# Kernel tuning notes

Measured on AMD Instinct MI355X. Metric: run time of the kernel, lower is better.

## Reference

```python
import jax, jax.numpy as jnp
import numpy as np

NUM_CLASSES = 7
B = 14336
D = 512
H_KDE = 0.2          # sklearn KernelDensity(bandwidth=0.2, kernel='gaussian')
KERNEL_MUL = 2.0
KERNEL_NUM = 5
BN_EPS = 1e-5


def _pairwise_sqdist(a, b):
    # ||a_i - b_j||^2 via gram trick; avoids the [n,n,d] broadcast tensor the torch code builds
    an = jnp.sum(a * a, axis=-1)
    bn = jnp.sum(b * b, axis=-1)
    d2 = an[:, None] + bn[None, :] - 2.0 * (a @ b.T)
    return jnp.maximum(d2, 0.0)


def _multi_kernel(total):
    # sum of KERNEL_NUM Gaussian kernels, bandwidths 1.25 * 2^i (bandwidth=5 / 2^(5//2))
    d2 = _pairwise_sqdist(total, total)
    bw0 = 5.0 / (KERNEL_MUL ** (KERNEL_NUM // 2))
    k = jnp.zeros_like(d2)
    for i in range(KERNEL_NUM):  # small fixed loop, avoids [5,n,n] intermediate
        k = k + jnp.exp(-d2 / (bw0 * (KERNEL_MUL ** i)))
    return k


def _mmd(src, tgt):
    m = src.shape[0]
    k = _multi_kernel(jnp.concatenate([src, tgt], axis=0))
    return jnp.mean(k[:m, :m] + k[m:, m:] - k[:m, m:] - k[m:, :m])


def _kde_weight(class_feats):
    # sklearn gaussian KDE: log p(x_i) = logsumexp_j(-||x_i-x_j||^2 / (2 h^2)) - log m - (d/2) log(2 pi h^2)
    # volume v = sum_i 1 / log p(x_i); weight = 1 / (v + 1e-5)
    C, m, d = class_feats.shape
    log_norm = -0.5 * d * jnp.log(2.0 * jnp.pi * (H_KDE ** 2)) - jnp.log(jnp.float32(m))

    def one(f):
        d2 = _pairwise_sqdist(f, f)
        logp = jax.nn.logsumexp(-d2 / (2.0 * (H_KDE ** 2)), axis=1) + log_norm
        return jnp.sum(1.0 / logp)

    v = jax.vmap(one)(class_feats)
    return 1.0 / (v + 1e-5)


def setup_inputs() -> dict:
    key = jax.random.key(0)
    k1, k2 = jax.random.split(key)
    fea = jax.random.normal(k1, (B, D), dtype=jnp.float32) * 0.05
    W_fc = jax.random.normal(k2, (NUM_CLASSES, D), dtype=jnp.float32) * 0.02
    gamma = jnp.ones((NUM_CLASSES,), dtype=jnp.float32)
    beta = jnp.zeros((NUM_CLASSES,), dtype=jnp.float32)
    # balanced, contiguous class blocks so per-class splits are static reshapes
    targets = jnp.repeat(jnp.arange(NUM_CLASSES, dtype=jnp.int32), B // NUM_CLASSES)
    return {"fea": fea, "W_fc": W_fc, "gamma": gamma, "beta": beta, "targets": targets}


def reference(fea, W_fc, gamma, beta, targets):
    Bn, d = fea.shape
    C = NUM_CLASSES
    m = Bn // C

    # out = BatchNorm1d(fc(fea)) in train mode (biased batch stats)
    logits = fea @ W_fc.T                              # [B, C]
    mu = jnp.mean(logits, axis=0)
    var = jnp.var(logits, axis=0)
    out = gamma * (logits - mu) / jnp.sqrt(var + BN_EPS) + beta

    # split_feature_makeLD with balanced contiguous targets -> static reshape
    cf = fea.reshape(C, m, d)                          # [C, m, D]

    # KDE density weights: computed on detached numpy features in the original -> stop_gradient
    w = jax.lax.stop_gradient(_kde_weight(cf))         # [C]

    def per_class(i):
        src = cf[i]
        # remove_element concatenates classes 0..i-1, i+1..C-1 in order;
        # first m rows of that = class 0 (class 1 when i == 0)
        tgt = cf[jnp.where(i > 0, 0, 1)]
        return _mmd(src, tgt)

    losses = jax.vmap(per_class)(jnp.arange(C))        # [C]
    affinity_loss = -jnp.sum(losses * w)
    return (out, affinity_loss)
```

## Files before the change

### kernel.cpp

```cpp
#include <hip/hip_runtime.h>

#define B_ROWS 14336
#define D_DIM  512
#define C_CLS  7
#define M_CLS  2048

typedef __attribute__((ext_vector_type(4))) float f32x4;

#define FP8_SCALE 64.0f
#define INV_2S2   (2.0f / 4096.0f)

typedef const __attribute__((address_space(1))) char gchar_t;
typedef __attribute__((address_space(3))) char lchar_t;

__device__ __forceinline__ void gload16(const char* g, char* l) {
  __builtin_amdgcn_global_load_lds((gchar_t*)g, (lchar_t*)l, 16, 0, 0);
}

__global__ __launch_bounds__(256) void k_prep(const float* __restrict__ fea,
                                              const float* __restrict__ W,
                                              char* __restrict__ f8p,
                                              float* __restrict__ an,
                                              float* __restrict__ logits,
                                              float* __restrict__ zb) {
  int t = threadIdx.x, wave = t >> 6, lane = t & 63;
  if (blockIdx.x == 0 && t < 64) zb[t] = 0.f;
  __shared__ char lrow[16 * 528];

  int r0 = blockIdx.x * 16;
#pragma unroll
  for (int k = 0; k < 4; ++k) {
    int rl = wave * 4 + k;
    int row = r0 + rl;
    const float4* fr4 = (const float4*)(fea + (size_t)row * D_DIM);
    float4 v0 = fr4[lane * 2], v1 = fr4[lane * 2 + 1];

    float p[8];
#pragma unroll
    for (int c = 0; c < 7; ++c) {
      const float4* w4 = (const float4*)(W + c * D_DIM);
      float4 q0 = w4[lane * 2], q1 = w4[lane * 2 + 1];
      p[c] = v0.x * q0.x + v0.y * q0.y + v0.z * q0.z + v0.w * q0.w +
             v1.x * q1.x + v1.y * q1.y + v1.z * q1.z + v1.w * q1.w;
    }
    p[7] = v0.x * v0.x + v0.y * v0.y + v0.z * v0.z + v0.w * v0.w +
           v1.x * v1.x + v1.y * v1.y + v1.z * v1.z + v1.w * v1.w;

#pragma unroll
    for (int c = 0; c < 8; ++c) {
      p[c] += __shfl_xor(p[c], 1);
      p[c] += __shfl_xor(p[c], 2);
      p[c] += __shfl_xor(p[c], 4);
    }
    int v = lane & 7;
    float y = p[0];
    y = (v == 1) ? p[1] : y;
    y = (v == 2) ? p[2] : y;
    y = (v == 3) ? p[3] : y;
    y = (v == 4) ? p[4] : y;
    y = (v == 5) ? p[5] : y;
    y = (v == 6) ? p[6] : y;
    y = (v == 7) ? p[7] : y;
    y += __shfl_xor(y, 8);
    y += __shfl_xor(y, 16);
    y += __shfl_xor(y, 32);
    if (lane < 7) logits[row * 7 + lane] = y;
    else if (lane == 7) an[row] = y;

    int w0 = __builtin_amdgcn_cvt_pk_fp8_f32(v0.x * FP8_SCALE, v0.y * FP8_SCALE, 0, 0);
    w0     = __builtin_amdgcn_cvt_pk_fp8_f32(v0.z * FP8_SCALE, v0.w * FP8_SCALE, w0, 1);
    int w1 = __builtin_amdgcn_cvt_pk_fp8_f32(v1.x * FP8_SCALE, v1.y * FP8_SCALE, 0, 0);
    w1     = __builtin_amdgcn_cvt_pk_fp8_f32(v1.z * FP8_SCALE, v1.w * FP8_SCALE, w1, 1);
    *(int2*)&lrow[rl * 528 + lane * 8] = make_int2(w0, w1);
  }
  __syncthreads();
  int4* outp = (int4*)f8p + (size_t)blockIdx.x * 512;
#pragma unroll
  for (int pi = 0; pi < 2; ++pi) {
    int idx = pi * 256 + t;
    int kp = idx >> 6, l = idx & 63;
    int sr = l & 15, qk = l >> 4;
    int2 lo = *(const int2*)&lrow[sr * 528 + kp * 64 + qk * 8];
    int2 hi = *(const int2*)&lrow[sr * 528 + kp * 64 + 32 + qk * 8];
    outp[idx] = make_int4(lo.x, lo.y, hi.x, hi.y);
  }
}

__global__ __launch_bounds__(256, 4) void k_gram(const char* __restrict__ f8p,
                                                 const float* __restrict__ an,
                                                 const float* __restrict__ logits,
                                                 float* __restrict__ S,
                                                 float* __restrict__ rs_part,
                                                 float* __restrict__ S1,
                                                 float* __restrict__ S2,
                                                 float* __restrict__ aff) {
  int x = blockIdx.x & 7, u = blockIdx.x >> 3;
  int t = threadIdx.x, lane = t & 63, wave = t >> 6;
  if (blockIdx.x == 0 && t == 0) aff[0] = 0.f;

  if (u >= 311) {
    int blk;
    if (u == 311) blk = x;
    else { if (x >= 6) return; blk = 8 + x; }
    int idx = blk * 4 + wave;
    int c = idx >> 3, seg = idx & 7;
    int r0 = seg * 1792;
    float s1 = 0.f, s2 = 0.f;
    for (int j = lane; j < 1792; j += 64) {
      float v = logits[(size_t)(r0 + j) * 7 + c];
      s1 += v;
      s2 += v * v;
    }
#pragma unroll
    for (int o = 1; o < 64; o <<= 1) {
      s1 += __shfl_xor(s1, o);
      s2 += __shfl_xor(s2, o);
    }
    if (lane == 0) { atomicAdd(&S1[c], s1); atomicAdd(&S2[c], s2); }
    return;
  }

  int cls1, cls2, ti, tj, Sidx;
  bool self;
  if (x < 7 && u < 136) {
    int a = 0, r = u;
    while (r > a) { r -= a + 1; ++a; }
    ti = a; tj = r;
    cls1 = x; cls2 = x; Sidx = x; self = true;
  } else {
    int j;
    if (x < 7) j = x * 175 + (u - 136);
    else j = 1225 + u;
    int p = j >> 8, t256 = j & 255;
    ti = t256 >> 4; tj = t256 & 15;
    cls1 = p + 1; cls2 = 0; Sidx = 7 + p; self = false;
  }

  __shared__ char ldsA[2][8192];
  __shared__ char ldsB[2][8192];
  __shared__ float bacc[4];

  int R0 = cls1 * 2048 + ti * 128;
  int C0 = cls2 * 2048 + tj * 128;

  const char* gA0 = f8p + ((size_t)(R0 >> 4) + wave * 2)     * 8192 + lane * 16;
  const char* gA1 = f8p + ((size_t)(R0 >> 4) + wave * 2 + 1) * 8192 + lane * 16;
  const char* gB0 = f8p + ((size_t)(C0 >> 4) + wave * 2)     * 8192 + lane * 16;
  const char* gB1 = f8p + ((size_t)(C0 >> 4) + wave * 2 + 1) * 8192 + lane * 16;

  int wr = wave >> 1, wc = wave & 1;
  int q = lane >> 4, s = lane & 15;

  f32x4 acc[4][4];
#pragma unroll
  for (int i = 0; i < 4; ++i)
#pragma unroll
    for (int j = 0; j < 4; ++j)
      acc[i][j] = (f32x4){0.f, 0.f, 0.f, 0.f};

  gload16(gA0, &ldsA[0][(wave * 2) * 1024 + lane * 16]);
  gload16(gA1, &ldsA[0][(wave * 2 + 1) * 1024 + lane * 16]);
  gload16(gB0, &ldsB[0][(wave * 2) * 1024 + lane * 16]);
  gload16(gB1, &ldsB[0][(wave * 2 + 1) * 1024 + lane * 16]);
  __syncthreads();

#define MM16(A0_, A1_, I0_, I1_)                                              \
  do {                                                                        \
    asm volatile("s_waitcnt lgkmcnt(0)" ::: "memory");                        \
    __builtin_amdgcn_sched_barrier(0);                                        \
    __builtin_amdgcn_s_setprio(1);                                            \
    _Pragma("unroll")                                                         \
    for (int j_ = 0; j_ < 4; ++j_)                                            \
      acc[I0_][j_] = __builtin_amdgcn_mfma_f32_16x16x32_fp8_fp8(              \
          A0_.x, bb[j_].x, acc[I0_][j_], 0, 0, 0);                            \
    _Pragma("unroll")                                                         \
    for (int j_ = 0; j_ < 4; ++j_)                                            \
      acc[I1_][j_] = __builtin_amdgcn_mfma_f32_16x16x32_fp8_fp8(              \
          A1_.x, bb[j_].x, acc[I1_][j_], 0, 0, 0);                            \
    _Pragma("unroll")                                                         \
    for (int j_ = 0; j_ < 4; ++j_)                                            \
      acc[I0_][j_] = __builtin_amdgcn_mfma_f32_16x16x32_fp8_fp8(              \
          A0_.y, bb[j_].y, acc[I0_][j_], 0, 0, 0);                            \
    _Pragma("unroll")                                                         \
    for (int j_ = 0; j_ < 4; ++j_)                                            \
      acc[I1_][j_] = __builtin_amdgcn_mfma_f32_16x16x32_fp8_fp8(              \
          A1_.y, bb[j_].y, acc[I1_][j_], 0, 0, 0);                            \
    __builtin_amdgcn_s_setprio(0);                                            \
  } while (0)

#pragma unroll 1
  for (int kt = 0; kt < 8; ++kt) {
    int cur = kt & 1;
    const char* LA = &ldsA[cur][(wr * 4) * 1024 + lane * 16];
    const char* LB = &ldsB[cur][(wc * 4) * 1024 + lane * 16];
    longlong2 a0, a1, bb[4];
    a0 = *(const longlong2*)(LA);
    a1 = *(const longlong2*)(LA + 1024);
#pragma unroll
    for (int j = 0; j < 4; ++j) bb[j] = *(const longlong2*)(LB + j * 1024);
    if (kt < 7) {
      int nb = cur ^ 1;
      gload16(gA0 + (kt + 1) * 1024, &ldsA[nb][(wave * 2) * 1024 + lane * 16]);
      gload16(gA1 + (kt + 1) * 1024, &ldsA[nb][(wave * 2 + 1) * 1024 + lane * 16]);
    }
    MM16(a0, a1, 0, 1);
    a0 = *(const longlong2*)(LA + 2 * 1024);
    a1 = *(const longlong2*)(LA + 3 * 1024);
    if (kt < 7) {
      int nb = cur ^ 1;
      gload16(gB0 + (kt + 1) * 1024, &ldsB[nb][(wave * 2) * 1024 + lane * 16]);
      gload16(gB1 + (kt + 1) * 1024, &ldsB[nb][(wave * 2 + 1) * 1024 + lane * 16]);
    }
    __builtin_amdgcn_s_barrier();
    asm volatile("" ::: "memory");
    MM16(a0, a1, 2, 3);
    if (kt < 7)
      asm volatile("s_waitcnt vmcnt(0)" ::: "memory");
    __builtin_amdgcn_s_barrier();
    asm volatile("" ::: "memory");
  }
#undef MM16

  bool dg = self && (ti == tj);
  bool mirror = self && (ti > tj);
  float blockAcc = 0.f;
  float colAcc[4] = {0.f, 0.f, 0.f, 0.f};
  float anB_[4];
#pragma unroll
  for (int j = 0; j < 4; ++j) anB_[j] = an[C0 + wc * 64 + j * 16 + s];

#pragma unroll
  for (int i = 0; i < 4; ++i) {
    f32x4 anA_ = *(const f32x4*)&an[R0 + wr * 64 + i * 16 + q * 4];
#pragma unroll
    for (int rg = 0; rg < 4; ++rg) {
      int rl = wr * 64 + i * 16 + q * 4 + rg;
      float aA = anA_[rg];
      float rowAcc = 0.f;
#pragma unroll
      for (int j = 0; j < 4; ++j) {
        int cl = wc * 64 + j * 16 + s;
        float g = acc[i][j][rg];
        float d2 = fmaxf(aA + anB_[j] - g * INV_2S2, 0.f);
        if (dg && rl == cl) d2 = 0.f;
        float e1 = __expf(-0.05f * d2);
        float e2 = e1 * e1, e4 = e2 * e2, e8 = e4 * e4, e16 = e8 * e8;
        blockAcc += e1 + e2 + e4 + e8 + e16;
        if (self) {
          float ek = __expf(-12.5f * d2);
          rowAcc += ek;
          if (mirror) colAcc[j] += ek;
        }
      }
      if (self) {
        rowAcc += __shfl_xor(rowAcc, 1);
        rowAcc += __shfl_xor(rowAcc, 2);
        rowAcc += __shfl_xor(rowAcc, 4);
        rowAcc += __shfl_xor(rowAcc, 8);
        if (s == 0)
          rs_part[(size_t)(R0 + rl) * 64 + tj * 2 + wc] = rowAcc;
      }
    }
  }
  if (mirror) {
#pragma unroll
    for (int j = 0; j < 4; ++j) {
      float v = colAcc[j];
      v += __shfl_xor(v, 16);
      v += __shfl_xor(v, 32);
      if (q == 0)
        rs_part[(size_t)(C0 + wc * 64 + j * 16 + s) * 64 + 32 + ti * 2 + wr] = v;
    }
    blockAcc *= 2.f;
  }
#pragma unroll
  for (int o = 1; o < 64; o <<= 1) blockAcc += __shfl_xor(blockAcc, o);
  if (lane == 0) bacc[wave] = blockAcc;
  __syncthreads();
  if (t == 0)
    atomicAdd(&S[Sidx], bacc[0] + bacc[1] + bacc[2] + bacc[3]);
}

__global__ __launch_bounds__(1024) void k_final(const float* __restrict__ logits,
                                                const float* __restrict__ S1,
                                                const float* __restrict__ S2,
                                                const float* __restrict__ gamma,
                                                const float* __restrict__ beta,
                                                const float* __restrict__ rs_part,
                                                const float* __restrict__ S,
                                                float* __restrict__ out) {
  int b = blockIdx.x, t = threadIdx.x;
  if (b < 98) {
    int idx = b * 1024 + t;
    int row = idx / 7;
    int c = idx - row * 7;
    float mu = S1[c] * (1.f / 14336.f);
    float var = S2[c] * (1.f / 14336.f) - mu * mu;
    out[idx] = gamma[c] * (logits[idx] - mu) * rsqrtf(var + 1e-5f) + beta[c];
    return;
  }
  int c = b - 98;
  const float LOG_NORM = 345.9110632f;
  float v = 0.f;
  for (int i = t; i < M_CLS; i += 1024) {
    int bi = i >> 7;
    const float* rp = rs_part + (size_t)(c * M_CLS + i) * 64;
    float rsum = 0.f;
    const float2* rpd = (const float2*)rp;
    for (int k = 0; k <= bi; ++k) {
      float2 xx = rpd[k];
      rsum += xx.x + xx.y;
    }
    const float2* rpm = (const float2*)(rp + 34 + 2 * bi);
    for (int k = 0; k < 15 - bi; ++k) {
      float2 xx = rpm[k];
      rsum += xx.x + xx.y;
    }
    v += 1.f / (logf(rsum) + LOG_NORM);
  }
#pragma unroll
  for (int o = 1; o < 64; o <<= 1) v += __shfl_xor(v, o);
  __shared__ float r[16];
  if ((t & 63) == 0) r[t >> 6] = v;
  __syncthreads();
  if (t == 0) {
    float vs = 0.f;
#pragma unroll
    for (int w = 0; w < 16; ++w) vs += r[w];
    float w = 1.f / (vs + 1e-5f);
    const float inv_m2 = 1.0f / ((float)M_CLS * (float)M_CLS);
    float Ssrc = S[c];
    float Stgt = (c > 0) ? S[0] : S[1];
    float X    = (c > 0) ? S[6 + c] : S[7];
    float mmd = (Ssrc + Stgt - 2.f * X) * inv_m2;
    atomicAdd(&out[100352], -mmd * w);
  }
}

extern "C" void kernel_launch(void* const* d_in, const int* in_sizes, int n_in,
                              void* d_out, int out_size, void* d_ws, size_t ws_size,
                              hipStream_t stream) {
  const float* fea   = (const float*)d_in[0];
  const float* W_fc  = (const float*)d_in[1];
  const float* gamma = (const float*)d_in[2];
  const float* beta  = (const float*)d_in[3];
  float* out = (float*)d_out;

  char* ws = (char*)d_ws;
  char* f8p = ws;
  float* fbase   = (float*)(ws + 7340032);
  float* an      = fbase;
  float* logits  = fbase + 14336;
  float* zb      = fbase + 114688;
  float* S1      = zb;
  float* S2      = zb + 7;
  float* S       = zb + 16;
  float* rs_part = fbase + 114752;

  k_prep <<<896,  256, 0, stream>>>(fea, W_fc, f8p, an, logits, zb);
  k_gram <<<2504, 256, 0, stream>>>(f8p, an, logits, S, rs_part, S1, S2,
                                    out + 100352);
  k_final<<<105, 1024, 0, stream>>>(logits, S1, S2, gamma, beta, rs_part, S, out);
}
```

Measured before the change: 157.7 us.

## Fuse final reduction kernel into gram kernel using atomic-counter spin waits

Removes the separate k_final launch. Its work now runs in 105 extra blocks appended to k_gram, which spin on global atomic counters until the BN-stat blocks or all gram blocks have finished. This saves one kernel launch and lets the BN normalization overlap with the gram tail. In exchange it depends on the counters being zeroed by k_prep and on the waiting blocks not starving producer blocks of residency, which risks deadlock or wasted CU slots. The KDE/MMD epilogue now runs with 256 threads per class instead of 1024.

Result: slower. 274.2 us (+73.9%).

```diff
diff --git a/kernel.cpp b/kernel.cpp
--- a/kernel.cpp
+++ b/kernel.cpp
@@ -93,15 +93,88 @@
                                                  float* __restrict__ rs_part,
                                                  float* __restrict__ S1,
                                                  float* __restrict__ S2,
-                                                 float* __restrict__ aff) {
+                                                 const float* __restrict__ gamma,
+                                                 const float* __restrict__ beta,
+                                                 float* __restrict__ out) {
+  int t = threadIdx.x, lane = t & 63, wave = t >> 6;
+  unsigned* cntg = (unsigned*)(S1 + 60);
+  unsigned* cntb = (unsigned*)(S1 + 61);
+
+  __shared__ char ldsA[2][8192];
+  __shared__ char ldsB[2][8192];
+  __shared__ float bacc[4];
+
+  if (blockIdx.x >= 2504) {
+    int fid = blockIdx.x - 2504;
+    if (fid < 98) {
+      if (t == 0)
+        while (atomicAdd(cntb, 0u) < 14u) __builtin_amdgcn_s_sleep(32);
+      __syncthreads();
+      __threadfence();
+#pragma unroll
+      for (int k = 0; k < 4; ++k) {
+        int idx = fid * 1024 + k * 256 + t;
+        int row = idx / 7;
+        int c = idx - row * 7;
+        float mu = S1[c] * (1.f / 14336.f);
+        float var = S2[c] * (1.f / 14336.f) - mu * mu;
+        out[idx] = gamma[c] * (logits[idx] - mu) * rsqrtf(var + 1e-5f) + beta[c];
+      }
+      return;
+    }
+    int c = fid - 98;
+    if (t == 0)
+      while (atomicAdd(cntg, 0u) < 2504u) __builtin_amdgcn_s_sleep(32);
+    __syncthreads();
+    __threadfence();
+    const float LOG_NORM = 345.9110632f;
+    float v = 0.f;
+    for (int i = t; i < M_CLS; i += 256) {
+      int bi = i >> 7;
+      const float* rp = rs_part + (size_t)(c * M_CLS + i) * 64;
+      float rsum = 0.f;
+      const float2* rpd = (const float2*)rp;
+      for (int k = 0; k <= bi; ++k) {
+        float2 xx = rpd[k];
+        rsum += xx.x + xx.y;
+      }
+      const float2* rpm = (const float2*)(rp + 34 + 2 * bi);
+      for (int k = 0; k < 15 - bi; ++k) {
+        float2 xx = rpm[k];
+        rsum += xx.x + xx.y;
+      }
+      v += 1.f / (logf(rsum) + LOG_NORM);
+    }
+#pragma unroll
+    for (int o = 1; o < 64; o <<= 1) v += __shfl_xor(v, o);
+    if (lane == 0) bacc[wave] = v;
+    __syncthreads();
+    if (t == 0) {
+      float vs = bacc[0] + bacc[1] + bacc[2] + bacc[3];
+      float w = 1.f / (vs + 1e-5f);
+      const float inv_m2 = 1.0f / ((float)M_CLS * (float)M_CLS);
+      float Ssrc = S[c];
+      float Stgt = (c > 0) ? S[0] : S[1];
+      float X    = (c > 0) ? S[6 + c] : S[7];
+      float mmd = (Ssrc + Stgt - 2.f * X) * inv_m2;
+      atomicAdd(&out[100352], -mmd * w);
+    }
+    return;
+  }
+
   int x = blockIdx.x & 7, u = blockIdx.x >> 3;
-  int t = threadIdx.x, lane = t & 63, wave = t >> 6;
-  if (blockIdx.x == 0 && t == 0) aff[0] = 0.f;
+  if (blockIdx.x == 0 && t == 0) out[100352] = 0.f;
 
   if (u >= 311) {
     int blk;
     if (u == 311) blk = x;
-    else { if (x >= 6) return; blk = 8 + x; }
+    else {
+      if (x >= 6) {
+        if (t == 0) atomicAdd(cntg, 1u);
+        return;
+      }
+      blk = 8 + x;
+    }
     int idx = blk * 4 + wave;
     int c = idx >> 3, seg = idx & 7;
     int r0 = seg * 1792;
@@ -117,6 +190,12 @@
       s2 += __shfl_xor(s2, o);
     }
     if (lane == 0) { atomicAdd(&S1[c], s1); atomicAdd(&S2[c], s2); }
+    __syncthreads();
+    if (t == 0) {
+      __threadfence();
+      atomicAdd(cntb, 1u);
+      atomicAdd(cntg, 1u);
+    }
     return;
   }
 
@@ -135,10 +214,6 @@
     ti = t256 >> 4; tj = t256 & 15;
     cls1 = p + 1; cls2 = 0; Sidx = 7 + p; self = false;
   }
-
-  __shared__ char ldsA[2][8192];
-  __shared__ char ldsB[2][8192];
-  __shared__ float bacc[4];
 
   int R0 = cls1 * 2048 + ti * 128;
   int C0 = cls2 * 2048 + tj * 128;
@@ -277,63 +352,10 @@
   for (int o = 1; o < 64; o <<= 1) blockAcc += __shfl_xor(blockAcc, o);
   if (lane == 0) bacc[wave] = blockAcc;
   __syncthreads();
-  if (t == 0)
+  if (t == 0) {
     atomicAdd(&S[Sidx], bacc[0] + bacc[1] + bacc[2] + bacc[3]);
-}
-
-__global__ __launch_bounds__(1024) void k_final(const float* __restrict__ logits,
-                                                const float* __restrict__ S1,
-                                                const float* __restrict__ S2,
-                                                const float* __restrict__ gamma,
-                                                const float* __restrict__ beta,
-                                                const float* __restrict__ rs_part,
-                                                const float* __restrict__ S,
-                                                float* __restrict__ out) {
-  int b = blockIdx.x, t = threadIdx.x;
-  if (b < 98) {
-    int idx = b * 1024 + t;
-    int row = idx / 7;
-    int c = idx - row * 7;
-    float mu = S1[c] * (1.f / 14336.f);
-    float var = S2[c] * (1.f / 14336.f) - mu * mu;
-    out[idx] = gamma[c] * (logits[idx] - mu) * rsqrtf(var + 1e-5f) + beta[c];
-    return;
-  }
-  int c = b - 98;
-  const float LOG_NORM = 345.9110632f;
-  float v = 0.f;
-  for (int i = t; i < M_CLS; i += 1024) {
-    int bi = i >> 7;
-    const float* rp = rs_part + (size_t)(c * M_CLS + i) * 64;
-    float rsum = 0.f;
-    const float2* rpd = (const float2*)rp;
-    for (int k = 0; k <= bi; ++k) {
-      float2 xx = rpd[k];
-      rsum += xx.x + xx.y;
-    }
-    const float2* rpm = (const float2*)(rp + 34 + 2 * bi);
-    for (int k = 0; k < 15 - bi; ++k) {
-      float2 xx = rpm[k];
-      rsum += xx.x + xx.y;
-    }
-    v += 1.f / (logf(rsum) + LOG_NORM);
-  }
-#pragma unroll
-  for (int o = 1; o < 64; o <<= 1) v += __shfl_xor(v, o);
-  __shared__ float r[16];
-  if ((t & 63) == 0) r[t >> 6] = v;
-  __syncthreads();
-  if (t == 0) {
-    float vs = 0.f;
-#pragma unroll
-    for (int w = 0; w < 16; ++w) vs += r[w];
-    float w = 1.f / (vs + 1e-5f);
-    const float inv_m2 = 1.0f / ((float)M_CLS * (float)M_CLS);
-    float Ssrc = S[c];
-    float Stgt = (c > 0) ? S[0] : S[1];
-    float X    = (c > 0) ? S[6 + c] : S[7];
-    float mmd = (Ssrc + Stgt - 2.f * X) * inv_m2;
-    atomicAdd(&out[100352], -mmd * w);
+    __threadfence();
+    atomicAdd(cntg, 1u);
   }
 }
 
@@ -358,7 +380,6 @@
   float* rs_part = fbase + 114752;
 
   k_prep <<<896,  256, 0, stream>>>(fea, W_fc, f8p, an, logits, zb);
-  k_gram <<<2504, 256, 0, stream>>>(f8p, an, logits, S, rs_part, S1, S2,
-                                    out + 100352);
-  k_final<<<105, 1024, 0, stream>>>(logits, S1, S2, gamma, beta, rs_part, S, out);
+  k_gram <<<2609, 256, 0, stream>>>(f8p, an, logits, S, rs_part, S1, S2,
+                                    gamma, beta, out);
 }
```
